# Optimization experiments

Hardware: AMD Instinct MI355X
Metric: run time of the kernel (lower is better)

Reference implementation:

```python
import jax, jax.numpy as jnp
import numpy as np

NUM_HEADS = 16


def setup_inputs() -> dict:
    key = jax.random.key(0)
    k1, k2, k3 = jax.random.split(key, 3)
    B, N, D = 4, 1024, 1024
    x = jax.random.normal(k1, (B, N, D), dtype=jnp.float32)
    w_qkv = jax.random.normal(k2, (3 * D, D), dtype=jnp.float32) * (D ** -0.5)
    w_out = jax.random.normal(k3, (D, D), dtype=jnp.float32) * (D ** -0.5)
    b_out = jnp.zeros((D,), dtype=jnp.float32)
    return {"x": x, "w_qkv": w_qkv, "w_out": w_out, "b_out": b_out}


def reference(x, w_qkv, w_out, b_out):
    B, N, D = x.shape
    H = NUM_HEADS
    d = D // H
    scale = d ** -0.5
    # qkv projection (no bias): [B,N,3D] -> [B,N,3,H,d]
    qkv = jnp.einsum('bnd,ed->bne', x, w_qkv).reshape(B, N, 3, H, d)
    # -> [3, B, H, N, d]
    qkv = jnp.transpose(qkv, (2, 0, 3, 1, 4))
    q, k, v = qkv[0], qkv[1], qkv[2]
    # attention scores [B,H,N,N], stable softmax
    scores = jnp.einsum('bhqd,bhkd->bhqk', q, k) * scale
    attn = jax.nn.softmax(scores, axis=-1)
    out = jnp.einsum('bhqk,bhkd->bhqd', attn, v)  # [B,H,N,d]
    out = jnp.transpose(out, (0, 2, 1, 3)).reshape(B, N, D)
    # output projection with bias
    return jnp.einsum('bnd,ed->bne', out, w_out) + b_out
```

## Files before the change

kernel.cpp:

```cpp
#include <hip/hip_runtime.h>
#include <stdint.h>

typedef __bf16 bf16_t;
typedef bf16_t bf16x8 __attribute__((ext_vector_type(8)));
typedef float f32x4 __attribute__((ext_vector_type(4)));

static __device__ __forceinline__ unsigned short f2bf(float f) {
    union { float f; unsigned int u; } v; v.f = f;
    unsigned int u = v.u;
    unsigned int r = (u + 0x7fffu + ((u >> 16) & 1u)) >> 16;
    return (unsigned short)r;
}

static __device__ __forceinline__ bf16x8 as_frag(uint4 v) {
    union { uint4 u; bf16x8 b; } c; c.u = v; return c.b;
}

#define MFMA16(a, b, c) __builtin_amdgcn_mfma_f32_16x16x32_bf16((a), (b), (c), 0, 0, 0)

__global__ void cvt_all(const float* __restrict__ x,
                        const float* __restrict__ wq,
                        const float* __restrict__ wo,
                        unsigned short* __restrict__ xb,
                        unsigned short* __restrict__ wqb,
                        unsigned short* __restrict__ wob) {
    const float* in; unsigned short* out; int n4;
    if (blockIdx.y == 0)      { in = x;  out = xb;  n4 = 1048576; }
    else if (blockIdx.y == 1) { in = wq; out = wqb; n4 = 786432; }
    else                      { in = wo; out = wob; n4 = 262144; }
    for (int i = blockIdx.x * 256 + threadIdx.x; i < n4; i += 1024 * 256) {
        float4 v = ((const float4*)in)[i];
        ushort4 o;
        o.x = f2bf(v.x); o.y = f2bf(v.y); o.z = f2bf(v.z); o.w = f2bf(v.w);
        ((ushort4*)out)[i] = o;
    }
}

template <int OUTMODE>
__global__ __launch_bounds__(256, 2) void gemm_bt(
    const unsigned short* __restrict__ A,
    const unsigned short* __restrict__ B,
    void* __restrict__ Cv,
    const float* __restrict__ bias,
    unsigned short* __restrict__ Vt,
    int M, int N, int K) {
    __shared__ uint4 As[8 * 128];
    __shared__ uint4 Bs[8 * 128];
    const int tid  = threadIdx.x;
    const int lane = tid & 63;
    const int wave = tid >> 6;
    const int quad = lane >> 4;
    const int l16  = lane & 15;
    const int wr   = (wave >> 1) * 64;
    const int wc   = (wave & 1) * 64;
    const int bm   = blockIdx.y * 128;
    const int bn   = blockIdx.x * 128;

    f32x4 zero4 = {0.f, 0.f, 0.f, 0.f};
    f32x4 acc[4][4];
#pragma unroll
    for (int mt = 0; mt < 4; ++mt)
#pragma unroll
        for (int nt = 0; nt < 4; ++nt) acc[mt][nt] = zero4;

    for (int k0 = 0; k0 < K; k0 += 64) {
        __syncthreads();
#pragma unroll
        for (int i = 0; i < 4; ++i) {
            int s = i * 256 + tid;
            int kc = s & 7, row = s >> 3;
            As[kc * 128 + (row ^ (kc << 1))] =
                *(const uint4*)(A + (size_t)(bm + row) * K + k0 + kc * 8);
            Bs[kc * 128 + (row ^ (kc << 1))] =
                *(const uint4*)(B + (size_t)(bn + row) * K + k0 + kc * 8);
        }
        __syncthreads();
#pragma unroll
        for (int ks = 0; ks < 2; ++ks) {
            int kc = ks * 4 + quad;
            bf16x8 af[4], bff[4];
#pragma unroll
            for (int mt = 0; mt < 4; ++mt) {
                int row = wr + mt * 16 + l16;
                af[mt] = as_frag(As[kc * 128 + (row ^ (kc << 1))]);
            }
#pragma unroll
            for (int nt = 0; nt < 4; ++nt) {
                int row = wc + nt * 16 + l16;
                bff[nt] = as_frag(Bs[kc * 128 + (row ^ (kc << 1))]);
            }
#pragma unroll
            for (int mt = 0; mt < 4; ++mt)
#pragma unroll
                for (int nt = 0; nt < 4; ++nt)
                    acc[mt][nt] = MFMA16(af[mt], bff[nt], acc[mt][nt]);
        }
    }

    if (OUTMODE == 1) {
        float* C = (float*)Cv;
#pragma unroll
        for (int mt = 0; mt < 4; ++mt)
#pragma unroll
            for (int nt = 0; nt < 4; ++nt) {
                int col = bn + wc + nt * 16 + l16;
                float bv = bias ? bias[col] : 0.f;
#pragma unroll
                for (int r = 0; r < 4; ++r) {
                    int row = bm + wr + mt * 16 + quad * 4 + r;
                    C[(size_t)row * N + col] = acc[mt][nt][r] + bv;
                }
            }
    } else if (OUTMODE == 0) {
        unsigned short* C = (unsigned short*)Cv;
#pragma unroll
        for (int mt = 0; mt < 4; ++mt)
#pragma unroll
            for (int nt = 0; nt < 4; ++nt) {
                int col = bn + wc + nt * 16 + l16;
#pragma unroll
                for (int r = 0; r < 4; ++r) {
                    int row = bm + wr + mt * 16 + quad * 4 + r;
                    C[(size_t)row * N + col] = f2bf(acc[mt][nt][r]);
                }
            }
    } else {
        if (bn < 2048) {
            unsigned short* C = (unsigned short*)Cv;
#pragma unroll
            for (int mt = 0; mt < 4; ++mt)
#pragma unroll
                for (int nt = 0; nt < 4; ++nt) {
                    int col = bn + wc + nt * 16 + l16;
#pragma unroll
                    for (int r = 0; r < 4; ++r) {
                        int row = bm + wr + mt * 16 + quad * 4 + r;
                        C[(size_t)row * 2048 + col] = f2bf(acc[mt][nt][r]);
                    }
                }
        } else {
#pragma unroll
            for (int mt = 0; mt < 4; ++mt)
#pragma unroll
                for (int nt = 0; nt < 4; ++nt) {
                    int col = bn + wc + nt * 16 + l16 - 2048;
                    int h = col >> 6, dd = col & 63;
                    int token0 = bm + wr + mt * 16 + quad * 4;
                    int b = token0 >> 10, t = token0 & 1023;
                    ushort4 pk;
                    pk.x = f2bf(acc[mt][nt][0]);
                    pk.y = f2bf(acc[mt][nt][1]);
                    pk.z = f2bf(acc[mt][nt][2]);
                    pk.w = f2bf(acc[mt][nt][3]);
                    *(ushort4*)(Vt + ((size_t)((b * 16 + h) * 64 + dd) * 1024 + t)) = pk;
                }
        }
    }
}

__global__ __launch_bounds__(512, 4) void attn_kernel(
    const unsigned short* __restrict__ qk,
    const unsigned short* __restrict__ vt,
    unsigned short* __restrict__ out) {
    __shared__ uint4 Ps[8 * 128];
    __shared__ uint4 Ks[2][8 * 64];
    __shared__ uint4 Vs[2][8 * 64];

    const int tid  = threadIdx.x;
    const int lane = tid & 63;
    const int wave = tid >> 6;
    const int quad = lane >> 4;
    const int l16  = lane & 15;
    const int bh   = blockIdx.x;
    const int b    = bh >> 4, h = bh & 15;
    const int qbase = blockIdx.y * 128;
    const size_t rowbase = (size_t)b * 1024;
    const int hoff = h * 64;
    const float c1 = 0.125f * 1.44269504088896f;

#pragma unroll
    for (int i = 0; i < 2; ++i) {
        int s = i * 512 + tid;
        int kc = s & 7, row = s >> 3;
        Ps[kc * 128 + (row ^ (kc << 1))] =
            *(const uint4*)(qk + (rowbase + qbase + row) * 2048 + hoff + kc * 8);
    }
    __syncthreads();
    bf16x8 qf[2];
#pragma unroll
    for (int ks = 0; ks < 2; ++ks) {
        int kc = ks * 4 + quad;
        int row = wave * 16 + l16;
        qf[ks] = as_frag(Ps[kc * 128 + (row ^ (kc << 1))]);
    }

    f32x4 zero4 = {0.f, 0.f, 0.f, 0.f};
    f32x4 Oacc[4];
#pragma unroll
    for (int no = 0; no < 4; ++no) Oacc[no] = zero4;
    float mcur = -1e30f, lcur = 0.f;

    const int kc_t = tid & 7, r_t = tid >> 3;
    const unsigned short* kptr = qk + (rowbase + r_t) * 2048 + 1024 + hoff + kc_t * 8;
    const unsigned short* vptr = vt + ((size_t)bh * 64 + r_t) * 1024 + kc_t * 8;
    const int ksl = kc_t * 64 + (r_t ^ (kc_t << 1));

    uint4 kreg = *(const uint4*)(kptr);
    uint4 vreg = *(const uint4*)(vptr);

    for (int kt = 0; kt < 16; ++kt) {
        const int buf = kt & 1;
        Ks[buf][ksl] = kreg;
        Vs[buf][ksl] = vreg;
        if (kt < 15) {
            kreg = *(const uint4*)(kptr + (kt + 1) * 64 * 2048);
            vreg = *(const uint4*)(vptr + (kt + 1) * 64);
        }
        __syncthreads();

        f32x4 st[4];
#pragma unroll
        for (int nt = 0; nt < 4; ++nt) st[nt] = zero4;
#pragma unroll
        for (int ks = 0; ks < 2; ++ks) {
            int kc = ks * 4 + quad;
            bf16x8 kf[4];
#pragma unroll
            for (int nt = 0; nt < 4; ++nt) {
                int row = nt * 16 + l16;
                kf[nt] = as_frag(Ks[buf][kc * 64 + (row ^ (kc << 1))]);
            }
#pragma unroll
            for (int nt = 0; nt < 4; ++nt)
                st[nt] = MFMA16(kf[nt], qf[ks], st[nt]);
        }

        float mx = st[0][0];
#pragma unroll
        for (int nt = 0; nt < 4; ++nt)
#pragma unroll
            for (int r = 0; r < 4; ++r) mx = fmaxf(mx, st[nt][r]);
        mx = fmaxf(mx, __shfl_xor(mx, 16, 64));
        mx = fmaxf(mx, __shfl_xor(mx, 32, 64));
        float mnew = fmaxf(mcur, mx);
        float al = __builtin_amdgcn_exp2f(c1 * (mcur - mnew));
        mcur = mnew;
        float rs = 0.f;
        const int q = wave * 16 + l16;
#pragma unroll
        for (int nt = 0; nt < 4; ++nt) {
            ushort4 pk;
            float p0 = __builtin_amdgcn_exp2f(c1 * (st[nt][0] - mnew));
            float p1 = __builtin_amdgcn_exp2f(c1 * (st[nt][1] - mnew));
            float p2 = __builtin_amdgcn_exp2f(c1 * (st[nt][2] - mnew));
            float p3 = __builtin_amdgcn_exp2f(c1 * (st[nt][3] - mnew));
            rs += (p0 + p1) + (p2 + p3);
            pk.x = f2bf(p0); pk.y = f2bf(p1); pk.z = f2bf(p2); pk.w = f2bf(p3);
            int c = nt * 4 + quad, kc = c >> 1;
            ((uint2*)Ps)[(kc * 128 + (q ^ (kc << 1))) * 2 + (c & 1)] = *(uint2*)&pk;
        }
        rs += __shfl_xor(rs, 16, 64);
        rs += __shfl_xor(rs, 32, 64);
        lcur = lcur * al + rs;

#pragma unroll
        for (int r = 0; r < 4; ++r) {
            float aO = __shfl(al, quad * 4 + r, 64);
#pragma unroll
            for (int no = 0; no < 4; ++no) Oacc[no][r] *= aO;
        }

#pragma unroll
        for (int kstep = 0; kstep < 2; ++kstep) {
            int kc = kstep * 4 + quad;
            bf16x8 pf = as_frag(Ps[kc * 128 + ((wave * 16 + l16) ^ (kc << 1))]);
            bf16x8 vf[4];
#pragma unroll
            for (int no = 0; no < 4; ++no) {
                int dd = no * 16 + l16;
                vf[no] = as_frag(Vs[buf][kc * 64 + (dd ^ (kc << 1))]);
            }
#pragma unroll
            for (int no = 0; no < 4; ++no)
                Oacc[no] = MFMA16(pf, vf[no], Oacc[no]);
        }
    }

    float linv = 1.f / lcur;
#pragma unroll
    for (int r = 0; r < 4; ++r) {
        float iv = __shfl(linv, quad * 4 + r, 64);
        int qrow = qbase + wave * 16 + quad * 4 + r;
#pragma unroll
        for (int no = 0; no < 4; ++no) {
            int dd = no * 16 + l16;
            out[(rowbase + qrow) * 1024 + hoff + dd] = f2bf(Oacc[no][r] * iv);
        }
    }
}

extern "C" void kernel_launch(void* const* d_in, const int* in_sizes, int n_in,
                              void* d_out, int out_size, void* d_ws, size_t ws_size,
                              hipStream_t stream) {
    const float* x     = (const float*)d_in[0];
    const float* w_qkv = (const float*)d_in[1];
    const float* w_out = (const float*)d_in[2];
    const float* b_out = (const float*)d_in[3];

    char* ws = (char*)d_ws;
    unsigned short* wqkvb = (unsigned short*)(ws);
    unsigned short* woutb = (unsigned short*)(ws + 6291456);
    unsigned short* qkb   = (unsigned short*)(ws + 8388608);
    unsigned short* vtb   = (unsigned short*)(ws + 25165824);
    unsigned short* xb    = (unsigned short*)(ws + 33554432);
    unsigned short* attnb = xb;

    cvt_all<<<dim3(1024, 3), 256, 0, stream>>>(x, w_qkv, w_out, xb, wqkvb, woutb);

    gemm_bt<2><<<dim3(24, 32), 256, 0, stream>>>(xb, wqkvb, (void*)qkb, nullptr,
                                                 vtb, 4096, 3072, 1024);
    attn_kernel<<<dim3(64, 8), 512, 0, stream>>>(qkb, vtb, attnb);
    gemm_bt<1><<<dim3(8, 32), 256, 0, stream>>>(attnb, woutb, d_out, b_out,
                                                nullptr, 4096, 1024, 1024);
}
```

Before: 173.3 us.

## Use direct global-to-LDS loads for GEMM and attention K/V tiles

Replaces the register-staged global loads followed by LDS stores with `__builtin_amdgcn_global_load_lds` 16-byte transfers. This applies to both the GEMM A/B tiles and the attention K/V double buffers. The LDS layout becomes row-major with an XOR swizzle on the k-chunk index, and the fragment reads are updated to match. In the attention kernel, the next tile is prefetched asynchronously into the alternate buffer after a barrier at the top of each iteration. The aim is to cut VGPR pressure and the instructions spent copying through registers. The cost is a reliance on barriers and wait counts correctly covering the asynchronous LDS writes.

```diff
diff --git a/kernel.cpp b/kernel.cpp
--- a/kernel.cpp
+++ b/kernel.cpp
@@ -14,6 +14,12 @@
 
 static __device__ __forceinline__ bf16x8 as_frag(uint4 v) {
     union { uint4 u; bf16x8 b; } c; c.u = v; return c.b;
+}
+
+static __device__ __forceinline__ void gl2lds16(const unsigned short* g, uint4* l) {
+    __builtin_amdgcn_global_load_lds(
+        (const __attribute__((address_space(1))) unsigned int*)g,
+        (__attribute__((address_space(3))) unsigned int*)l, 16, 0, 0);
 }
 
 #define MFMA16(a, b, c) __builtin_amdgcn_mfma_f32_16x16x32_bf16((a), (b), (c), 0, 0, 0)
@@ -44,8 +50,8 @@
     const float* __restrict__ bias,
     unsigned short* __restrict__ Vt,
     int M, int N, int K) {
-    __shared__ uint4 As[8 * 128];
-    __shared__ uint4 Bs[8 * 128];
+    __shared__ uint4 As[1024];
+    __shared__ uint4 Bs[1024];
     const int tid  = threadIdx.x;
     const int lane = tid & 63;
     const int wave = tid >> 6;
@@ -63,16 +69,18 @@
 #pragma unroll
         for (int nt = 0; nt < 4; ++nt) acc[mt][nt] = zero4;
 
+    const int s_row = tid >> 3;
+    const int s_kcs = tid & 7;
+
     for (int k0 = 0; k0 < K; k0 += 64) {
         __syncthreads();
 #pragma unroll
         for (int i = 0; i < 4; ++i) {
-            int s = i * 256 + tid;
-            int kc = s & 7, row = s >> 3;
-            As[kc * 128 + (row ^ (kc << 1))] =
-                *(const uint4*)(A + (size_t)(bm + row) * K + k0 + kc * 8);
-            Bs[kc * 128 + (row ^ (kc << 1))] =
-                *(const uint4*)(B + (size_t)(bn + row) * K + k0 + kc * 8);
+            int s   = i * 256 + tid;
+            int row = i * 32 + s_row;
+            int kcg = s_kcs ^ (row & 7);
+            gl2lds16(A + (size_t)(bm + row) * K + k0 + kcg * 8, &As[s]);
+            gl2lds16(B + (size_t)(bn + row) * K + k0 + kcg * 8, &Bs[s]);
         }
         __syncthreads();
 #pragma unroll
@@ -82,12 +90,12 @@
 #pragma unroll
             for (int mt = 0; mt < 4; ++mt) {
                 int row = wr + mt * 16 + l16;
-                af[mt] = as_frag(As[kc * 128 + (row ^ (kc << 1))]);
+                af[mt] = as_frag(As[row * 8 + (kc ^ (row & 7))]);
             }
 #pragma unroll
             for (int nt = 0; nt < 4; ++nt) {
                 int row = wc + nt * 16 + l16;
-                bff[nt] = as_frag(Bs[kc * 128 + (row ^ (kc << 1))]);
+                bff[nt] = as_frag(Bs[row * 8 + (kc ^ (row & 7))]);
             }
 #pragma unroll
             for (int mt = 0; mt < 4; ++mt)
@@ -163,8 +171,8 @@
     const unsigned short* __restrict__ vt,
     unsigned short* __restrict__ out) {
     __shared__ uint4 Ps[8 * 128];
-    __shared__ uint4 Ks[2][8 * 64];
-    __shared__ uint4 Vs[2][8 * 64];
+    __shared__ uint4 Ks[2][512];
+    __shared__ uint4 Vs[2][512];
 
     const int tid  = threadIdx.x;
     const int lane = tid & 63;
@@ -178,6 +186,14 @@
     const int hoff = h * 64;
     const float c1 = 0.125f * 1.44269504088896f;
 
+    const int st_row = tid >> 3;
+    const int st_kcg = (tid & 7) ^ (st_row & 7);
+    const unsigned short* kp0 = qk + (rowbase)*2048 + 1024 + hoff;
+    const unsigned short* vp0 = vt + (size_t)bh * 65536;
+
+    gl2lds16(kp0 + (size_t)st_row * 2048 + st_kcg * 8, &Ks[0][tid]);
+    gl2lds16(vp0 + (size_t)st_row * 1024 + st_kcg * 8, &Vs[0][tid]);
+
 #pragma unroll
     for (int i = 0; i < 2; ++i) {
         int s = i * 512 + tid;
@@ -200,23 +216,15 @@
     for (int no = 0; no < 4; ++no) Oacc[no] = zero4;
     float mcur = -1e30f, lcur = 0.f;
 
-    const int kc_t = tid & 7, r_t = tid >> 3;
-    const unsigned short* kptr = qk + (rowbase + r_t) * 2048 + 1024 + hoff + kc_t * 8;
-    const unsigned short* vptr = vt + ((size_t)bh * 64 + r_t) * 1024 + kc_t * 8;
-    const int ksl = kc_t * 64 + (r_t ^ (kc_t << 1));
-
-    uint4 kreg = *(const uint4*)(kptr);
-    uint4 vreg = *(const uint4*)(vptr);
-
     for (int kt = 0; kt < 16; ++kt) {
         const int buf = kt & 1;
-        Ks[buf][ksl] = kreg;
-        Vs[buf][ksl] = vreg;
+        if (kt) __syncthreads();
         if (kt < 15) {
-            kreg = *(const uint4*)(kptr + (kt + 1) * 64 * 2048);
-            vreg = *(const uint4*)(vptr + (kt + 1) * 64);
-        }
-        __syncthreads();
+            gl2lds16(kp0 + (size_t)((kt + 1) * 64 + st_row) * 2048 + st_kcg * 8,
+                     &Ks[buf ^ 1][tid]);
+            gl2lds16(vp0 + (size_t)st_row * 1024 + (kt + 1) * 64 + st_kcg * 8,
+                     &Vs[buf ^ 1][tid]);
+        }
 
         f32x4 st[4];
 #pragma unroll
@@ -228,7 +236,7 @@
 #pragma unroll
             for (int nt = 0; nt < 4; ++nt) {
                 int row = nt * 16 + l16;
-                kf[nt] = as_frag(Ks[buf][kc * 64 + (row ^ (kc << 1))]);
+                kf[nt] = as_frag(Ks[buf][row * 8 + (kc ^ (row & 7))]);
             }
 #pragma unroll
             for (int nt = 0; nt < 4; ++nt)
@@ -278,7 +286,7 @@
 #pragma unroll
             for (int no = 0; no < 4; ++no) {
                 int dd = no * 16 + l16;
-                vf[no] = as_frag(Vs[buf][kc * 64 + (dd ^ (kc << 1))]);
+                vf[no] = as_frag(Vs[buf][dd * 8 + (kc ^ (dd & 7))]);
             }
 #pragma unroll
             for (int no = 0; no < 4; ++no)
```

Result: faster. 168.7 us (-2.6%).
